# Kernel tuning notes

Measured on AMD Instinct MI355X. Metric: run time of the kernel, lower is better.

The kernel has to match this reference:

```python
import jax, jax.numpy as jnp
import numpy as np

N = 50000        # num nodes
E = 1_000_000    # num edges
F_IN = 256       # input feature dim
UNITS = 128      # hidden units
NUM_CLASSES = 40 # output classes
EPS = 1e-3       # Keras BatchNormalization default epsilon


def setup_inputs() -> dict:
    key = jax.random.key(0)
    ks = jax.random.split(key, 32)
    inp = {
        "x": jax.random.normal(ks[0], (N, F_IN), jnp.float32),
        "edge_index": jax.random.randint(ks[1], (2, E), 0, N, jnp.int32),
        "edge_weight": jax.random.uniform(ks[2], (E,), jnp.float32),
    }
    dims = [(F_IN, UNITS), (UNITS, UNITS), (UNITS, NUM_CLASSES)]
    ki = 3
    for li, (fi, fo) in enumerate(dims, 1):
        inp[f"w_gcn{li}"] = jax.random.normal(ks[ki], (fi, fo), jnp.float32) / np.sqrt(fi).astype(np.float32); ki += 1
        inp[f"w_self{li}"] = jax.random.normal(ks[ki], (fi, fo), jnp.float32) / np.sqrt(fi).astype(np.float32); ki += 1
        inp[f"b{li}"] = jnp.zeros((fo,), jnp.float32)
        inp[f"gamma{li}"] = 1.0 + 0.1 * jax.random.normal(ks[ki], (fo,), jnp.float32); ki += 1
        inp[f"beta{li}"] = 0.1 * jax.random.normal(ks[ki], (fo,), jnp.float32); ki += 1
        inp[f"mean{li}"] = 0.1 * jax.random.normal(ks[ki], (fo,), jnp.float32); ki += 1
        inp[f"var{li}"] = jnp.ones((fo,), jnp.float32)
    return inp


def _gcn_bs(h, src, dst, norm_w, w_gcn, w_self, b, gamma, beta, mean, var, act):
    # GCN aggregation: transform then gather->weight->scatter-sum
    hw = h @ w_gcn                                   # [N, out]
    msg = hw[src] * norm_w[:, None]                  # [E, out]
    agg = jax.ops.segment_sum(msg, dst, num_segments=N)
    out = agg + h @ w_self + b                       # self-loop dense + bias
    # BatchNorm (inference: moving stats)
    out = (out - mean) * jax.lax.rsqrt(var + EPS) * gamma + beta
    return act(out) if act is not None else out


def reference(x, edge_index, edge_weight,
              w_gcn1, w_self1, b1, gamma1, beta1, mean1, var1,
              w_gcn2, w_self2, b2, gamma2, beta2, mean2, var2,
              w_gcn3, w_self3, b3, gamma3, beta3, mean3, var3):
    src, dst = edge_index[0], edge_index[1]
    # symmetric GCN normalization (renorm=False: no added self loops)
    deg = jax.ops.segment_sum(edge_weight, dst, num_segments=N)
    dinv = jnp.where(deg > 0, jax.lax.rsqrt(jnp.where(deg > 0, deg, 1.0)), 0.0)
    norm_w = dinv[src] * edge_weight * dinv[dst]
    # inference: DropEdge and Dropout are identity
    h = _gcn_bs(x, src, dst, norm_w, w_gcn1, w_self1, b1, gamma1, beta1, mean1, var1, jax.nn.relu)
    h = _gcn_bs(h, src, dst, norm_w, w_gcn2, w_self2, b2, gamma2, beta2, mean2, var2, jax.nn.relu)
    h = _gcn_bs(h, src, dst, norm_w, w_gcn3, w_self3, b3, gamma3, beta3, mean3, var3, None)
    return h
```

## Files before the change

kernel.cpp:

```cpp
#include <hip/hip_runtime.h>
#include <hip/hip_bf16.h>

#define NN 50000
#define EE 1000000
static constexpr float EPSV = 1e-3f;
static constexpr float FIXSCALE = 131072.f;

typedef __attribute__((ext_vector_type(8))) short short8;
typedef __attribute__((ext_vector_type(4))) float fx4;

__device__ inline float blo(unsigned u) { return __uint_as_float(u << 16); }
__device__ inline float bhi(unsigned u) { return __uint_as_float(u & 0xffff0000u); }
__device__ inline unsigned short f2b(float f) {
    __hip_bfloat16 h = __float2bfloat16(f);
    return *(unsigned short*)&h;
}
__device__ inline unsigned pack2(float a, float b) {
    return (unsigned)f2b(a) | ((unsigned)f2b(b) << 16);
}

__device__ inline void gload_lds16(const unsigned short* g, unsigned short* ldsbase) {
    __builtin_amdgcn_global_load_lds(
        (const __attribute__((address_space(1))) unsigned int*)(const void*)g,
        (__attribute__((address_space(3))) unsigned int*)(void*)ldsbase, 16, 0, 0);
}


#define ZB 196
#define WB1 256
#define WB2 128
#define WB3 64
#define XB 12500

__global__ void setupx_kernel(unsigned* __restrict__ cnt32,
                              const float* __restrict__ wg1, const float* __restrict__ ws1,
                              unsigned short* __restrict__ Wt1,
                              const float* __restrict__ wg2, const float* __restrict__ ws2,
                              unsigned short* __restrict__ Wt2,
                              const float* __restrict__ wg3, const float* __restrict__ ws3,
                              unsigned short* __restrict__ Wt3,
                              const float4* __restrict__ x, uint2* __restrict__ xb) {
    int b = blockIdx.x;
    int t = threadIdx.x;
    if (b < ZB) {
        int i = b * 256 + t;
        if (i < NN) cnt32[i] = 0u;
    } else if (b < ZB + WB1) {
        int idx = (b - ZB) * 256 + t;
        int n = idx >> 8, k = idx & 255;
        float v = (n < 128) ? wg1[(size_t)k * 128 + n]
                            : ws1[(size_t)k * 128 + (n - 128)];
        Wt1[idx] = f2b(v);
    } else if (b < ZB + WB1 + WB2) {
        int idx = (b - ZB - WB1) * 256 + t;
        int n = idx >> 7, k = idx & 127;
        float v = (n < 128) ? wg2[(size_t)k * 128 + n]
                            : ws2[(size_t)k * 128 + (n - 128)];
        Wt2[idx] = f2b(v);
    } else if (b < ZB + WB1 + WB2 + WB3) {
        int idx = (b - ZB - WB1 - WB2) * 256 + t;
        int n = idx >> 7, k = idx & 127;
        float v = 0.f;
        if (n < 40) v = wg3[(size_t)k * 40 + n];
        else if (n < 80) v = ws3[(size_t)k * 40 + (n - 40)];
        Wt3[idx] = f2b(v);
    } else {
        int i = (b - ZB - WB1 - WB2 - WB3) * 256 + t;
        float4 v = x[i];
        xb[i] = make_uint2(pack2(v.x, v.y), pack2(v.z, v.w));
    }
}


__device__ __forceinline__ void gemm2ph_body(int bx, int by,
                                             const unsigned short* __restrict__ Ab,
                                             const unsigned short* __restrict__ Wt,
                                             const float* __restrict__ bias,
                                             unsigned short* __restrict__ Cg,
                                             unsigned short* __restrict__ Cs,
                                             int M, int K, int Fo,
                                             unsigned short* sA, unsigned short* sB) {
    const int t = threadIdx.x;
    const int lane = t & 63;
    const int wave = t >> 6;
    const int l15 = lane & 15, quad = lane >> 4;
    const int row0 = bx * 64;
    const int colbase = by * 128;

    fx4 acc[4][2];
#pragma unroll
    for (int r = 0; r < 4; ++r)
#pragma unroll
        for (int c = 0; c < 2; ++c) acc[r][c] = (fx4){0.f, 0.f, 0.f, 0.f};

    auto stage = [&](int kc, int half) {
        unsigned short* dA = sA + half * 2048;
        unsigned short* dB = sB + half * 4096;
#pragma unroll
        for (int j = 0; j < 3; ++j) {
            int o = wave * 3 + j;
            int ak = kc + quad * 8;
            if (o < 4) {
                int ar = row0 + o * 16 + l15;
                if (ar >= M) ar = M - 1;
                gload_lds16(Ab + (size_t)ar * K + ak, dA + o * 512);
            } else {
                int bo = o - 4;
                int br = colbase + bo * 16 + l15;
                gload_lds16(Wt + (size_t)br * K + ak, dB + bo * 512);
            }
        }
    };

    stage(0, 0);
    __syncthreads();
    const int nt = K >> 5;
    int cur = 0;
    for (int tt = 0; tt < nt; ++tt) {
        if (tt + 1 < nt) stage((tt + 1) * 32, cur ^ 1);
        const unsigned short* cA = sA + cur * 2048;
        const unsigned short* cB = sB + cur * 4096;
        short8 a[4], b[2];
#pragma unroll
        for (int r = 0; r < 4; ++r)
            a[r] = *reinterpret_cast<const short8*>(&cA[r * 512 + lane * 8]);
#pragma unroll
        for (int c = 0; c < 2; ++c)
            b[c] = *reinterpret_cast<const short8*>(&cB[(wave * 2 + c) * 512 + lane * 8]);
#pragma unroll
        for (int r = 0; r < 4; ++r)
#pragma unroll
            for (int c = 0; c < 2; ++c)
                acc[r][c] = __builtin_amdgcn_mfma_f32_16x16x32_bf16(a[r], b[c], acc[r][c], 0, 0, 0);
        __syncthreads();
        cur ^= 1;
    }

#pragma unroll
    for (int r = 0; r < 4; ++r) {
#pragma unroll
        for (int reg = 0; reg < 4; ++reg) {
            int row = row0 + r * 16 + quad * 4 + reg;
            if (row >= M) continue;
#pragma unroll
            for (int c = 0; c < 2; ++c) {
                int f = colbase + wave * 32 + c * 16 + l15;
                if (f >= 2 * Fo) continue;
                bool isG = (f < Fo);
                int col = isG ? f : f - Fo;
                float badd = isG ? 0.f : bias[col];
                unsigned short* basep = isG ? Cg : Cs;
                basep[(size_t)row * Fo + col] = f2b(acc[r][c][reg] + badd);
            }
        }
    }
}


#define AB 256
#define GX 782
#define GB 1564

__global__ __launch_bounds__(256) void mega_kernel(
    const int* __restrict__ ei, const float* __restrict__ ew,
    unsigned* __restrict__ cnt32, unsigned* __restrict__ rank,
    const unsigned short* __restrict__ xb, const unsigned short* __restrict__ Wt1,
    const float* __restrict__ bias1,
    unsigned short* __restrict__ Cg, unsigned short* __restrict__ Cs) {
    __shared__ unsigned short sA[2 * 64 * 32];
    __shared__ unsigned short sB[2 * 128 * 32];
    int b = blockIdx.x;
    if (b < AB) {
        int gtid = b * 256 + threadIdx.x;
#pragma unroll
        for (int g = 0; g < 2; ++g) {
            int d[8];
            unsigned fx[8];
            bool val[8];
#pragma unroll
            for (int j = 0; j < 8; ++j) {
                int e = (g * 8 + j) * 65536 + gtid;
                val[j] = (e < EE);
                if (val[j]) {
                    d[j] = ei[EE + e];
                    fx[j] = __float2uint_rn(ew[e] * FIXSCALE);
                }
            }
#pragma unroll
            for (int j = 0; j < 8; ++j) {
                if (val[j]) {
                    int e = (g * 8 + j) * 65536 + gtid;
                    unsigned old = atomicAdd(&cnt32[d[j]], 0x01000000u | fx[j]);
                    rank[e] = old >> 24;
                }
            }
        }
        return;
    }
    int gi = b - AB;
    int by = gi / GX;
    int bx = gi - by * GX;
    gemm2ph_body(bx, by, xb, Wt1, bias1, Cg, Cs, NN, 256, 128, sA, sB);
}


__global__ __launch_bounds__(1024) void dinvsum_kernel(const unsigned* __restrict__ cnt32,
                                                       float* __restrict__ dinv,
                                                       int* __restrict__ bsum) {
    __shared__ int s[1024];
    const int t = threadIdx.x;
    int idx = blockIdx.x * 1024 + t;
    unsigned cv = 0u;
    if (idx < NN) cv = cnt32[idx];
    float deg = (float)(cv & 0x00ffffffu) * (1.f / FIXSCALE);
    if (idx < NN) dinv[idx] = (deg > 0.f) ? rsqrtf(deg) : 0.f;
    s[t] = (int)(cv >> 24);
    __syncthreads();
#pragma unroll
    for (int off = 512; off > 0; off >>= 1) {
        if (t < off) s[t] += s[t + off];
        __syncthreads();
    }
    if (t == 0) bsum[blockIdx.x] = s[0];
}

__global__ __launch_bounds__(64) void scanB_kernel(const int* __restrict__ bsum,
                                                   int* __restrict__ bpre, int nb) {
    int t = threadIdx.x;
    int v = (t < nb) ? bsum[t] : 0;
    int own = v;
#pragma unroll
    for (int off = 1; off < 64; off <<= 1) {
        int u = __shfl_up(v, off);
        if (t >= off) v += u;
    }
    if (t < nb) bpre[t] = v - own;
}

__global__ __launch_bounds__(1024) void scanC_kernel(const unsigned* __restrict__ cnt32,
                                                     const int* __restrict__ bpre,
                                                     int* __restrict__ rowstart) {
    __shared__ int s[1024];
    const int t = threadIdx.x;
    int idx = blockIdx.x * 1024 + t;
    int v = (idx < NN) ? (int)(cnt32[idx] >> 24) : 0;
    s[t] = v;
    __syncthreads();
#pragma unroll
    for (int off = 1; off < 1024; off <<= 1) {
        int u = (t >= off) ? s[t - off] : 0;
        __syncthreads();
        s[t] += u;
        __syncthreads();
    }
    if (idx < NN) rowstart[idx] = s[t] - v + bpre[blockIdx.x];
    if (idx == 0) rowstart[NN] = EE;
}

__global__ void fill_kernel(const int* __restrict__ ei, const float* __restrict__ ew,
                            const float* __restrict__ dinv, const int* __restrict__ rowstart,
                            const unsigned* __restrict__ rank, unsigned* __restrict__ eprec4) {
    int e = blockIdx.x * blockDim.x + threadIdx.x;
    if (e >= EE) return;
    int s = ei[e], d = ei[EE + e];
    int idx = rowstart[d] + (int)rank[e];
    float w = dinv[s] * ew[e] * dinv[d];
    eprec4[idx] = ((unsigned)s << 16) | (unsigned)f2b(w);
}

__global__ __launch_bounds__(256) void gemm_mfma(const unsigned short* __restrict__ Ab,
                                                 const unsigned short* __restrict__ Wt,
                                                 const float* __restrict__ bias,
                                                 unsigned short* __restrict__ Cg,
                                                 unsigned short* __restrict__ Cs,
                                                 int M, int K, int Fo) {
    __shared__ unsigned short sA[2 * 64 * 32];
    __shared__ unsigned short sB[2 * 128 * 32];
    gemm2ph_body(blockIdx.x, blockIdx.y, Ab, Wt, bias, Cg, Cs, M, K, Fo, sA, sB);
}


template <bool RELU>
__global__ __launch_bounds__(256) void agg128_kernel(
    const int* __restrict__ rowstart, const unsigned* __restrict__ eprec4,
    const unsigned* __restrict__ hw, const unsigned* __restrict__ selfC,
    const float* __restrict__ g, const float* __restrict__ be,
    const float* __restrict__ mu, const float* __restrict__ va,
    unsigned* __restrict__ out) {
    int wave = threadIdx.x >> 6;
    int lane = threadIdx.x & 63;
    int n = blockIdx.x * 4 + wave;
    if (n >= NN) return;
    unsigned scp = selfC[n * 64 + lane];
    float acc0 = blo(scp), acc1 = bhi(scp);
    int beg = rowstart[n], end = rowstart[n + 1];
    int i = beg;

    if (i + 16 <= end) {
        unsigned e[16];
        {
            int ifl = __builtin_amdgcn_readfirstlane(i);
#pragma unroll
            for (int k = 0; k < 16; ++k) e[k] = eprec4[ifl + k];
        }
        for (; i + 32 <= end; i += 16) {
            unsigned v[16];
#pragma unroll
            for (int k = 0; k < 16; ++k) v[k] = hw[(e[k] >> 16) * 64u + lane];
            unsigned en[16];
            {
                int ifl = __builtin_amdgcn_readfirstlane(i + 16);
#pragma unroll
                for (int k = 0; k < 16; ++k) en[k] = eprec4[ifl + k];
            }
#pragma unroll
            for (int k = 0; k < 16; ++k) {
                float w = blo(e[k]);
                acc0 += blo(v[k]) * w;
                acc1 += bhi(v[k]) * w;
            }
#pragma unroll
            for (int k = 0; k < 16; ++k) e[k] = en[k];
        }
        unsigned v[16];
#pragma unroll
        for (int k = 0; k < 16; ++k) v[k] = hw[(e[k] >> 16) * 64u + lane];
#pragma unroll
        for (int k = 0; k < 16; ++k) {
            float w = blo(e[k]);
            acc0 += blo(v[k]) * w;
            acc1 += bhi(v[k]) * w;
        }
        i += 16;
    }
    for (; i + 4 <= end; i += 4) {
        unsigned e0 = eprec4[i], e1 = eprec4[i + 1], e2 = eprec4[i + 2], e3 = eprec4[i + 3];
        unsigned v0 = hw[(e0 >> 16) * 64u + lane];
        unsigned v1 = hw[(e1 >> 16) * 64u + lane];
        unsigned v2 = hw[(e2 >> 16) * 64u + lane];
        unsigned v3 = hw[(e3 >> 16) * 64u + lane];
        float w0 = blo(e0), w1 = blo(e1), w2 = blo(e2), w3 = blo(e3);
        acc0 += blo(v0) * w0; acc1 += bhi(v0) * w0;
        acc0 += blo(v1) * w1; acc1 += bhi(v1) * w1;
        acc0 += blo(v2) * w2; acc1 += bhi(v2) * w2;
        acc0 += blo(v3) * w3; acc1 += bhi(v3) * w3;
    }
    for (; i < end; ++i) {
        unsigned e = eprec4[i];
        unsigned v = hw[(e >> 16) * 64u + lane];
        float w = blo(e);
        acc0 += blo(v) * w; acc1 += bhi(v) * w;
    }
    float2 m2 = reinterpret_cast<const float2*>(mu)[lane];
    float2 v2f = reinterpret_cast<const float2*>(va)[lane];
    float2 g2 = reinterpret_cast<const float2*>(g)[lane];
    float2 b2 = reinterpret_cast<const float2*>(be)[lane];
    float r0 = (acc0 - m2.x) * rsqrtf(v2f.x + EPSV) * g2.x + b2.x;
    float r1 = (acc1 - m2.y) * rsqrtf(v2f.y + EPSV) * g2.y + b2.y;
    if (RELU) {
        r0 = fmaxf(r0, 0.f);
        r1 = fmaxf(r1, 0.f);
    }
    out[n * 64 + lane] = pack2(r0, r1);
}


__global__ __launch_bounds__(256) void agg40_kernel(
    const int* __restrict__ rowstart, const unsigned* __restrict__ eprec4,
    const unsigned* __restrict__ hw, const unsigned* __restrict__ selfC,
    const float* __restrict__ g, const float* __restrict__ be,
    const float* __restrict__ mu, const float* __restrict__ va,
    float* __restrict__ out) {
    int wave = threadIdx.x >> 6;
    int lane = threadIdx.x & 63;
    int n = blockIdx.x * 4 + wave;
    if (n >= NN) return;
    int grp = lane / 20;
    int fl = lane - grp * 20;
    float acc0 = 0.f, acc1 = 0.f;
    int beg = rowstart[n], end = rowstart[n + 1];
    if (grp < 3) {
        int i = beg + grp;
        for (; i + 9 < end; i += 12) {
            unsigned e0 = eprec4[i], e1 = eprec4[i + 3], e2 = eprec4[i + 6], e3 = eprec4[i + 9];
            unsigned v0 = hw[(e0 >> 16) * 20u + fl];
            unsigned v1 = hw[(e1 >> 16) * 20u + fl];
            unsigned v2 = hw[(e2 >> 16) * 20u + fl];
            unsigned v3 = hw[(e3 >> 16) * 20u + fl];
            float w0 = blo(e0), w1 = blo(e1), w2 = blo(e2), w3 = blo(e3);
            acc0 += blo(v0) * w0; acc1 += bhi(v0) * w0;
            acc0 += blo(v1) * w1; acc1 += bhi(v1) * w1;
            acc0 += blo(v2) * w2; acc1 += bhi(v2) * w2;
            acc0 += blo(v3) * w3; acc1 += bhi(v3) * w3;
        }
        for (; i < end; i += 3) {
            unsigned e = eprec4[i];
            unsigned v = hw[(e >> 16) * 20u + fl];
            float w = blo(e);
            acc0 += blo(v) * w;
            acc1 += bhi(v) * w;
        }
    }
    acc0 += __shfl(acc0, lane + 20) + __shfl(acc0, lane + 40);
    acc1 += __shfl(acc1, lane + 20) + __shfl(acc1, lane + 40);
    if (lane < 20) {
        int f0 = lane * 2;
        unsigned scp = selfC[n * 20 + lane];
        acc0 += blo(scp);
        acc1 += bhi(scp);
        float2 m2 = reinterpret_cast<const float2*>(mu)[lane];
        float2 v2f = reinterpret_cast<const float2*>(va)[lane];
        float2 g2 = reinterpret_cast<const float2*>(g)[lane];
        float2 b2 = reinterpret_cast<const float2*>(be)[lane];
        float r0 = (acc0 - m2.x) * rsqrtf(v2f.x + EPSV) * g2.x + b2.x;
        float r1 = (acc1 - m2.y) * rsqrtf(v2f.y + EPSV) * g2.y + b2.y;
        *reinterpret_cast<float2*>(&out[(size_t)n * 40 + f0]) = make_float2(r0, r1);
    }
}


extern "C" void kernel_launch(void* const* d_in, const int* in_sizes, int n_in,
                              void* d_out, int out_size, void* d_ws, size_t ws_size,
                              hipStream_t stream) {
    const float* x = (const float*)d_in[0];
    const int* ei = (const int*)d_in[1];
    const float* ew = (const float*)d_in[2];

    const float* wg[3]  = {(const float*)d_in[3],  (const float*)d_in[10], (const float*)d_in[17]};
    const float* wsf[3] = {(const float*)d_in[4],  (const float*)d_in[11], (const float*)d_in[18]};
    const float* bs[3]  = {(const float*)d_in[5],  (const float*)d_in[12], (const float*)d_in[19]};
    const float* gm[3]  = {(const float*)d_in[6],  (const float*)d_in[13], (const float*)d_in[20]};
    const float* bt[3]  = {(const float*)d_in[7],  (const float*)d_in[14], (const float*)d_in[21]};
    const float* mu[3]  = {(const float*)d_in[8],  (const float*)d_in[15], (const float*)d_in[22]};
    const float* vr[3]  = {(const float*)d_in[9],  (const float*)d_in[16], (const float*)d_in[23]};

    float* W = (float*)d_ws;
    float* dinv     = W + 100096;
    unsigned* rank  = (unsigned*)(W + 150144);
    int*   bsum     = (int*)(W + 1150144);
    int*   bpre     = (int*)(W + 1150208);
    int*   rowstart = (int*)(W + 1150272);
    unsigned* eprec4 = (unsigned*)(W + 1200384);
    unsigned short* Wt1 = (unsigned short*)(W + 2200384);
    unsigned short* Wt2 = (unsigned short*)(W + 2233152);
    unsigned short* Wt3 = (unsigned short*)(W + 2249536);
    unsigned short* xb  = (unsigned short*)(W + 2257728);
    unsigned short* bufH = (unsigned short*)(W + 2257728);
    unsigned short* bufHW = (unsigned short*)(W + 8657728);
    unsigned short* bufSb = (unsigned short*)(W + 11857728);
    unsigned* cnt32 = (unsigned*)(W + 15057728);

    const int B = 256;
    const int SB = 49;

    setupx_kernel<<<ZB + WB1 + WB2 + WB3 + XB, B, 0, stream>>>(
        cnt32, wg[0], wsf[0], Wt1, wg[1], wsf[1], Wt2, wg[2], wsf[2], Wt3,
        (const float4*)x, (uint2*)xb);

    mega_kernel<<<AB + GB, B, 0, stream>>>(ei, ew, cnt32, rank, xb, Wt1, bs[0],
                                           bufHW, bufSb);

    dinvsum_kernel<<<SB, 1024, 0, stream>>>(cnt32, dinv, bsum);
    scanB_kernel<<<1, 64, 0, stream>>>(bsum, bpre, SB);
    scanC_kernel<<<SB, 1024, 0, stream>>>(cnt32, bpre, rowstart);
    fill_kernel<<<(EE + B - 1) / B, B, 0, stream>>>(ei, ew, dinv, rowstart, rank, eprec4);

    const int aggGrid = (NN + 3) / 4;
    dim3 g2(GX, 2), g1(GX, 1);

    agg128_kernel<true><<<aggGrid, B, 0, stream>>>(rowstart, eprec4, (const unsigned*)bufHW,
                                                   (const unsigned*)bufSb, gm[0], bt[0], mu[0], vr[0],
                                                   (unsigned*)bufH);

    gemm_mfma<<<g2, B, 0, stream>>>(bufH, Wt2, bs[1], bufHW, bufSb, NN, 128, 128);
    agg128_kernel<true><<<aggGrid, B, 0, stream>>>(rowstart, eprec4, (const unsigned*)bufHW,
                                                   (const unsigned*)bufSb, gm[1], bt[1], mu[1], vr[1],
                                                   (unsigned*)bufH);

    gemm_mfma<<<g1, B, 0, stream>>>(bufH, Wt3, bs[2], bufHW, bufSb, NN, 128, 40);
    agg40_kernel<<<aggGrid, B, 0, stream>>>(rowstart, eprec4, (const unsigned*)bufHW,
                                            (const unsigned*)bufSb, gm[2], bt[2], mu[2], vr[2],
                                            (float*)d_out);
}
```

Measured before the change: 374.3 us.

## Split node range to overlap aggregation tail with next-layer GEMM head

Splits the nodes at a fixed boundary. Aggregation of the first half runs alone, then one fused launch aggregates the second half while GEMM blocks process the already finished first half. The remaining GEMM tiles follow in a separate launch. Outputs go to split buffers that gathers select per source row, so the tail imbalance of the aggregation and of the small GEMMs can overlap. It adds a per-gather branch and more launches, and it depends on carefully aliased workspace offsets. The degree-count atomics loop is also flattened into a single 16-wide batch.

New measurement: 406.6 us. 8.6% more time.

```diff
diff --git a/kernel.cpp b/kernel.cpp
--- a/kernel.cpp
+++ b/kernel.cpp
@@ -5,6 +5,12 @@
 #define EE 1000000
 static constexpr float EPSV = 1e-3f;
 static constexpr float FIXSCALE = 131072.f;
+
+#define NSPLIT 24960
+#define AGA 6240
+#define AGB 6260
+#define GHA 390
+#define GHB 392
 
 typedef __attribute__((ext_vector_type(8))) short short8;
 typedef __attribute__((ext_vector_type(4))) float fx4;
@@ -172,28 +178,21 @@
     int b = blockIdx.x;
     if (b < AB) {
         int gtid = b * 256 + threadIdx.x;
-#pragma unroll
-        for (int g = 0; g < 2; ++g) {
-            int d[8];
-            unsigned fx[8];
-            bool val[8];
-#pragma unroll
-            for (int j = 0; j < 8; ++j) {
-                int e = (g * 8 + j) * 65536 + gtid;
-                val[j] = (e < EE);
-                if (val[j]) {
-                    d[j] = ei[EE + e];
-                    fx[j] = __float2uint_rn(ew[e] * FIXSCALE);
-                }
+        int d[16];
+        unsigned fx[16];
+#pragma unroll
+        for (int j = 0; j < 16; ++j) {
+            int e = j * 65536 + gtid;
+            if (e < EE) {
+                d[j] = ei[EE + e];
+                fx[j] = __float2uint_rn(ew[e] * FIXSCALE);
             }
-#pragma unroll
-            for (int j = 0; j < 8; ++j) {
-                if (val[j]) {
-                    int e = (g * 8 + j) * 65536 + gtid;
-                    unsigned old = atomicAdd(&cnt32[d[j]], 0x01000000u | fx[j]);
-                    rank[e] = old >> 24;
-                }
-            }
+        }
+#pragma unroll
+        for (int j = 0; j < 16; ++j) {
+            int e = j * 65536 + gtid;
+            if (e < EE)
+                rank[e] = atomicAdd(&cnt32[d[j]], 0x01000000u | fx[j]) >> 24;
         }
         return;
     }
@@ -273,25 +272,29 @@
                                                  const float* __restrict__ bias,
                                                  unsigned short* __restrict__ Cg,
                                                  unsigned short* __restrict__ Cs,
-                                                 int M, int K, int Fo) {
+                                                 int M, int K, int Fo, int bx0) {
     __shared__ unsigned short sA[2 * 64 * 32];
     __shared__ unsigned short sB[2 * 128 * 32];
-    gemm2ph_body(blockIdx.x, blockIdx.y, Ab, Wt, bias, Cg, Cs, M, K, Fo, sA, sB);
-}
-
-
-template <bool RELU>
-__global__ __launch_bounds__(256) void agg128_kernel(
+    gemm2ph_body(blockIdx.x + bx0, blockIdx.y, Ab, Wt, bias, Cg, Cs, M, K, Fo, sA, sB);
+}
+
+
+template <bool SPLIT>
+__device__ __forceinline__ void agg_node(
+    int n, int lane,
     const int* __restrict__ rowstart, const unsigned* __restrict__ eprec4,
-    const unsigned* __restrict__ hw, const unsigned* __restrict__ selfC,
+    const unsigned* __restrict__ hwA, const unsigned* __restrict__ hwB,
+    const unsigned* __restrict__ scA, const unsigned* __restrict__ scB,
     const float* __restrict__ g, const float* __restrict__ be,
     const float* __restrict__ mu, const float* __restrict__ va,
     unsigned* __restrict__ out) {
-    int wave = threadIdx.x >> 6;
-    int lane = threadIdx.x & 63;
-    int n = blockIdx.x * 4 + wave;
-    if (n >= NN) return;
-    unsigned scp = selfC[n * 64 + lane];
+    auto gat = [&](unsigned rec) -> unsigned {
+        unsigned srow = rec >> 16;
+        const unsigned* hp = (!SPLIT || srow < (unsigned)NSPLIT) ? hwA : hwB;
+        return hp[srow * 64u + lane];
+    };
+    const unsigned* scb = (!SPLIT || n < NSPLIT) ? scA : scB;
+    unsigned scp = scb[n * 64 + lane];
     float acc0 = blo(scp), acc1 = bhi(scp);
     int beg = rowstart[n], end = rowstart[n + 1];
     int i = beg;
@@ -306,7 +309,7 @@
         for (; i + 32 <= end; i += 16) {
             unsigned v[16];
 #pragma unroll
-            for (int k = 0; k < 16; ++k) v[k] = hw[(e[k] >> 16) * 64u + lane];
+            for (int k = 0; k < 16; ++k) v[k] = gat(e[k]);
             unsigned en[16];
             {
                 int ifl = __builtin_amdgcn_readfirstlane(i + 16);
@@ -324,7 +327,7 @@
         }
         unsigned v[16];
 #pragma unroll
-        for (int k = 0; k < 16; ++k) v[k] = hw[(e[k] >> 16) * 64u + lane];
+        for (int k = 0; k < 16; ++k) v[k] = gat(e[k]);
 #pragma unroll
         for (int k = 0; k < 16; ++k) {
             float w = blo(e[k]);
@@ -335,10 +338,7 @@
     }
     for (; i + 4 <= end; i += 4) {
         unsigned e0 = eprec4[i], e1 = eprec4[i + 1], e2 = eprec4[i + 2], e3 = eprec4[i + 3];
-        unsigned v0 = hw[(e0 >> 16) * 64u + lane];
-        unsigned v1 = hw[(e1 >> 16) * 64u + lane];
-        unsigned v2 = hw[(e2 >> 16) * 64u + lane];
-        unsigned v3 = hw[(e3 >> 16) * 64u + lane];
+        unsigned v0 = gat(e0), v1 = gat(e1), v2 = gat(e2), v3 = gat(e3);
         float w0 = blo(e0), w1 = blo(e1), w2 = blo(e2), w3 = blo(e3);
         acc0 += blo(v0) * w0; acc1 += bhi(v0) * w0;
         acc0 += blo(v1) * w1; acc1 += bhi(v1) * w1;
@@ -347,7 +347,7 @@
     }
     for (; i < end; ++i) {
         unsigned e = eprec4[i];
-        unsigned v = hw[(e >> 16) * 64u + lane];
+        unsigned v = gat(e);
         float w = blo(e);
         acc0 += blo(v) * w; acc1 += bhi(v) * w;
     }
@@ -357,17 +357,59 @@
     float2 b2 = reinterpret_cast<const float2*>(be)[lane];
     float r0 = (acc0 - m2.x) * rsqrtf(v2f.x + EPSV) * g2.x + b2.x;
     float r1 = (acc1 - m2.y) * rsqrtf(v2f.y + EPSV) * g2.y + b2.y;
-    if (RELU) {
-        r0 = fmaxf(r0, 0.f);
-        r1 = fmaxf(r1, 0.f);
-    }
+    r0 = fmaxf(r0, 0.f);
+    r1 = fmaxf(r1, 0.f);
     out[n * 64 + lane] = pack2(r0, r1);
 }
 
-
+template <bool SPLIT>
+__global__ __launch_bounds__(256) void agg128_kernel(
+    const int* __restrict__ rowstart, const unsigned* __restrict__ eprec4,
+    const unsigned* __restrict__ hwA, const unsigned* __restrict__ hwB,
+    const unsigned* __restrict__ scA, const unsigned* __restrict__ scB,
+    const float* __restrict__ g, const float* __restrict__ be,
+    const float* __restrict__ mu, const float* __restrict__ va,
+    unsigned* __restrict__ out, int nbase) {
+    int n = nbase + blockIdx.x * 4 + (threadIdx.x >> 6);
+    if (n >= NN) return;
+    agg_node<SPLIT>(n, threadIdx.x & 63, rowstart, eprec4, hwA, hwB, scA, scB,
+                    g, be, mu, va, out);
+}
+
+template <bool SPLIT>
+__global__ __launch_bounds__(256) void aggemm_pipe_kernel(
+    const int* __restrict__ rowstart, const unsigned* __restrict__ eprec4,
+    const unsigned* __restrict__ hwA, const unsigned* __restrict__ hwB,
+    const unsigned* __restrict__ scA, const unsigned* __restrict__ scB,
+    const float* __restrict__ g, const float* __restrict__ be,
+    const float* __restrict__ mu, const float* __restrict__ va,
+    unsigned* __restrict__ outH,
+    const unsigned short* __restrict__ Ab, const unsigned short* __restrict__ Wt,
+    const float* __restrict__ bias,
+    unsigned short* __restrict__ Cg, unsigned short* __restrict__ Cs,
+    int K, int Fo) {
+    __shared__ unsigned short sA[2 * 64 * 32];
+    __shared__ unsigned short sB[2 * 128 * 32];
+    int b = blockIdx.x;
+    if (b < AGB) {
+        int n = NSPLIT + b * 4 + (threadIdx.x >> 6);
+        if (n >= NN) return;
+        agg_node<SPLIT>(n, threadIdx.x & 63, rowstart, eprec4, hwA, hwB, scA, scB,
+                        g, be, mu, va, outH);
+        return;
+    }
+    int gi = b - AGB;
+    int by = gi / GHA;
+    int bx = gi - by * GHA;
+    gemm2ph_body(bx, by, Ab, Wt, bias, Cg, Cs, NSPLIT, K, Fo, sA, sB);
+}
+
+
+template <bool SPLIT>
 __global__ __launch_bounds__(256) void agg40_kernel(
     const int* __restrict__ rowstart, const unsigned* __restrict__ eprec4,
-    const unsigned* __restrict__ hw, const unsigned* __restrict__ selfC,
+    const unsigned* __restrict__ hwA, const unsigned* __restrict__ hwB,
+    const unsigned* __restrict__ scA, const unsigned* __restrict__ scB,
     const float* __restrict__ g, const float* __restrict__ be,
     const float* __restrict__ mu, const float* __restrict__ va,
     float* __restrict__ out) {
@@ -377,16 +419,18 @@
     if (n >= NN) return;
     int grp = lane / 20;
     int fl = lane - grp * 20;
+    auto gat = [&](unsigned rec) -> unsigned {
+        unsigned srow = rec >> 16;
+        const unsigned* hp = (!SPLIT || srow < (unsigned)NSPLIT) ? hwA : hwB;
+        return hp[srow * 20u + fl];
+    };
     float acc0 = 0.f, acc1 = 0.f;
     int beg = rowstart[n], end = rowstart[n + 1];
     if (grp < 3) {
         int i = beg + grp;
         for (; i + 9 < end; i += 12) {
             unsigned e0 = eprec4[i], e1 = eprec4[i + 3], e2 = eprec4[i + 6], e3 = eprec4[i + 9];
-            unsigned v0 = hw[(e0 >> 16) * 20u + fl];
-            unsigned v1 = hw[(e1 >> 16) * 20u + fl];
-            unsigned v2 = hw[(e2 >> 16) * 20u + fl];
-            unsigned v3 = hw[(e3 >> 16) * 20u + fl];
+            unsigned v0 = gat(e0), v1 = gat(e1), v2 = gat(e2), v3 = gat(e3);
             float w0 = blo(e0), w1 = blo(e1), w2 = blo(e2), w3 = blo(e3);
             acc0 += blo(v0) * w0; acc1 += bhi(v0) * w0;
             acc0 += blo(v1) * w1; acc1 += bhi(v1) * w1;
@@ -395,7 +439,7 @@
         }
         for (; i < end; i += 3) {
             unsigned e = eprec4[i];
-            unsigned v = hw[(e >> 16) * 20u + fl];
+            unsigned v = gat(e);
             float w = blo(e);
             acc0 += blo(v) * w;
             acc1 += bhi(v) * w;
@@ -405,7 +449,8 @@
     acc1 += __shfl(acc1, lane + 20) + __shfl(acc1, lane + 40);
     if (lane < 20) {
         int f0 = lane * 2;
-        unsigned scp = selfC[n * 20 + lane];
+        const unsigned* scb = (!SPLIT || n < NSPLIT) ? scA : scB;
+        unsigned scp = scb[n * 20 + lane];
         acc0 += blo(scp);
         acc1 += bhi(scp);
         float2 m2 = reinterpret_cast<const float2*>(mu)[lane];
@@ -446,9 +491,18 @@
     unsigned short* Wt3 = (unsigned short*)(W + 2249536);
     unsigned short* xb  = (unsigned short*)(W + 2257728);
     unsigned short* bufH = (unsigned short*)(W + 2257728);
-    unsigned short* bufHW = (unsigned short*)(W + 8657728);
-    unsigned short* bufSb = (unsigned short*)(W + 11857728);
+    unsigned* hw2A = (unsigned*)(W + 5457728);
+    unsigned* sc2A = hw2A + (size_t)NSPLIT * 64;
+    unsigned short* Yhw = (unsigned short*)(W + 8657728);
+    unsigned short* Ysb = (unsigned short*)(W + 11857728);
     unsigned* cnt32 = (unsigned*)(W + 15057728);
+    unsigned short* hw3A = (unsigned short*)(W + 150144);
+    unsigned short* sc3A = (unsigned short*)(W + 150144 + 499200);
+
+    unsigned short* hw2Bc = Yhw - (size_t)NSPLIT * 128;
+    unsigned short* sc2Bc = Ysb - (size_t)NSPLIT * 128;
+    unsigned short* hw3Bc = Yhw - (size_t)NSPLIT * 40;
+    unsigned short* sc3Bc = Ysb - (size_t)NSPLIT * 40;
 
     const int B = 256;
     const int SB = 49;
@@ -458,27 +512,43 @@
         (const float4*)x, (uint2*)xb);
 
     mega_kernel<<<AB + GB, B, 0, stream>>>(ei, ew, cnt32, rank, xb, Wt1, bs[0],
-                                           bufHW, bufSb);
+                                           Yhw, Ysb);
 
     dinvsum_kernel<<<SB, 1024, 0, stream>>>(cnt32, dinv, bsum);
     scanB_kernel<<<1, 64, 0, stream>>>(bsum, bpre, SB);
     scanC_kernel<<<SB, 1024, 0, stream>>>(cnt32, bpre, rowstart);
     fill_kernel<<<(EE + B - 1) / B, B, 0, stream>>>(ei, ew, dinv, rowstart, rank, eprec4);
 
-    const int aggGrid = (NN + 3) / 4;
-    dim3 g2(GX, 2), g1(GX, 1);
-
-    agg128_kernel<true><<<aggGrid, B, 0, stream>>>(rowstart, eprec4, (const unsigned*)bufHW,
-                                                   (const unsigned*)bufSb, gm[0], bt[0], mu[0], vr[0],
-                                                   (unsigned*)bufH);
-
-    gemm_mfma<<<g2, B, 0, stream>>>(bufH, Wt2, bs[1], bufHW, bufSb, NN, 128, 128);
-    agg128_kernel<true><<<aggGrid, B, 0, stream>>>(rowstart, eprec4, (const unsigned*)bufHW,
-                                                   (const unsigned*)bufSb, gm[1], bt[1], mu[1], vr[1],
-                                                   (unsigned*)bufH);
-
-    gemm_mfma<<<g1, B, 0, stream>>>(bufH, Wt3, bs[2], bufHW, bufSb, NN, 128, 40);
-    agg40_kernel<<<aggGrid, B, 0, stream>>>(rowstart, eprec4, (const unsigned*)bufHW,
-                                            (const unsigned*)bufSb, gm[2], bt[2], mu[2], vr[2],
-                                            (float*)d_out);
-}
+    agg128_kernel<false><<<AGA, B, 0, stream>>>(
+        rowstart, eprec4, (const unsigned*)Yhw, (const unsigned*)Yhw,
+        (const unsigned*)Ysb, (const unsigned*)Ysb,
+        gm[0], bt[0], mu[0], vr[0], (unsigned*)bufH, 0);
+
+    aggemm_pipe_kernel<false><<<AGB + GHA * 2, B, 0, stream>>>(
+        rowstart, eprec4, (const unsigned*)Yhw, (const unsigned*)Yhw,
+        (const unsigned*)Ysb, (const unsigned*)Ysb,
+        gm[0], bt[0], mu[0], vr[0], (unsigned*)bufH,
+        bufH, Wt2, bs[1], (unsigned short*)hw2A, (unsigned short*)sc2A, 128, 128);
+
+    gemm_mfma<<<dim3(GHB, 2), B, 0, stream>>>(bufH, Wt2, bs[1], hw2Bc, sc2Bc,
+                                              NN, 128, 128, GHA);
+
+    agg128_kernel<true><<<AGA, B, 0, stream>>>(
+        rowstart, eprec4, hw2A, (const unsigned*)hw2Bc,
+        sc2A, (const unsigned*)sc2Bc,
+        gm[1], bt[1], mu[1], vr[1], (unsigned*)bufH, 0);
+
+    aggemm_pipe_kernel<true><<<AGB + GHA, B, 0, stream>>>(
+        rowstart, eprec4, hw2A, (const unsigned*)hw2Bc,
+        sc2A, (const unsigned*)sc2Bc,
+        gm[1], bt[1], mu[1], vr[1], (unsigned*)bufH,
+        bufH, Wt3, bs[2], hw3A, sc3A, 128, 40);
+
+    gemm_mfma<<<dim3(GHB, 1), B, 0, stream>>>(bufH, Wt3, bs[2], hw3Bc, sc3Bc,
+                                              NN, 128, 40, GHA);
+
+    agg40_kernel<true><<<(NN + 3) / 4, B, 0, stream>>>(
+        rowstart, eprec4, (const unsigned*)hw3A, (const unsigned*)hw3Bc,
+        (const unsigned*)sc3A, (const unsigned*)sc3Bc,
+        gm[2], bt[2], mu[2], vr[2], (float*)d_out);
+}
```
